# Kernel optimization log

Hardware: AMD Instinct MI355X
Metric: run time of the kernel (lower is better)

Reference implementation:

```python
import jax, jax.numpy as jnp
import numpy as np

B, T, L, H, I, W_OUT = 64, 512, 2, 512, 128, 32


def setup_inputs() -> dict:
    key = jax.random.key(0)
    ks = jax.random.split(key, 12)
    stdv = 1.0 / np.sqrt(H)
    u = lambda k, shape: jax.random.uniform(k, shape, jnp.float32, -stdv, stdv)
    return {
        "x": jax.random.normal(ks[0], (B, T, I), jnp.float32),
        "noise": jax.random.normal(ks[1], (B, T, L, H), jnp.float32) * 0.1,
        "W_ih0": u(ks[2], (H, I)),
        "W_ih1": u(ks[3], (H, H)),
        "W_hh0": u(ks[4], (H, H)),
        "W_hh1": u(ks[5], (H, H)),
        "b_ih0": u(ks[6], (H,)),
        "b_ih1": u(ks[7], (H,)),
        "b_hh0": u(ks[8], (H,)),
        "b_hh1": u(ks[9], (H,)),
        "fc_w": u(ks[10], (W_OUT, H)),
        "fc_b": u(ks[11], (W_OUT,)),
    }


def reference(x, noise, W_ih0, W_ih1, W_hh0, W_hh1, b_ih0, b_ih1, b_hh0, b_hh1, fc_w, fc_b):
    # Sequential two-layer tanh RNN; scan over time keeps hidden state resident.
    h0 = jnp.zeros((B, H), x.dtype)
    h1 = jnp.zeros((B, H), x.dtype)

    def step(carry, inp):
        h0, h1 = carry
        x_t, n_t = inp  # x_t: [B,I], n_t: [B,L,H]
        h0 = jnp.tanh(x_t @ W_ih0.T + b_ih0 + h0 @ W_hh0.T + b_hh0 + n_t[:, 0, :])
        h1 = jnp.tanh(h0 @ W_ih1.T + b_ih1 + h1 @ W_hh1.T + b_hh1 + n_t[:, 1, :])
        return (h0, h1), None

    # time-major scan inputs
    (h0, h1), _ = jax.lax.scan(step, (h0, h1), (jnp.swapaxes(x, 0, 1), jnp.swapaxes(noise, 0, 1)))
    return h1 @ fc_w.T + fc_b  # [B, wheel_len]
```

## Files before the change

kernel.cpp:

```cpp
#include <hip/hip_runtime.h>


#define T_STEPS 512
#define NBATCH  64
#define DRING   32
#define THR_LEAD 20

typedef _Float16 half2v __attribute__((ext_vector_type(2)));
typedef _Float16 f16x8  __attribute__((ext_vector_type(8)));
typedef float    f32x4  __attribute__((ext_vector_type(4)));

__device__ __forceinline__ unsigned pack2(float a, float b) {
    _Float16 fa = (_Float16)a, fb = (_Float16)b;
    unsigned short ua = __builtin_bit_cast(unsigned short, fa);
    unsigned short ub = __builtin_bit_cast(unsigned short, fb);
    return (unsigned)ua | ((unsigned)ub << 16);
}

__device__ __forceinline__ float fast_tanh(float xv) {
    float e2 = __builtin_amdgcn_exp2f(xv * 2.885390082f);
    return 1.f - 2.f * __builtin_amdgcn_rcpf(e2 + 1.f);
}

__device__ __forceinline__ f32x4 mfma16(uint4 a, uint4 b, f32x4 c) {
    return __builtin_amdgcn_mfma_f32_16x16x32_f16(
        __builtin_bit_cast(f16x8, a), __builtin_bit_cast(f16x8, b), c, 0, 0, 0);
}

__device__ __forceinline__ void bar_lgkm() {
    asm volatile("s_waitcnt lgkmcnt(0)\n\ts_barrier" ::: "memory");
}

__device__ __forceinline__ float ntload_f(const float* p) {
    return __builtin_nontemporal_load(p);
}
__device__ __forceinline__ float2 ntload_f2(const float* p) {
    float a = __builtin_nontemporal_load(p);
    float b = __builtin_nontemporal_load(p + 1);
    return make_float2(a, b);
}

__device__ __forceinline__ unsigned poll1(unsigned long long* p, unsigned tag,
                                          long& budget) {
    unsigned long long v = __hip_atomic_load(p, __ATOMIC_RELAXED, __HIP_MEMORY_SCOPE_AGENT);
    while ((unsigned)(v >> 32) != tag && budget > 0) {
        v = __hip_atomic_load(p, __ATOMIC_RELAXED, __HIP_MEMORY_SCOPE_AGENT);
        --budget;
    }
    return (unsigned)v;
}

__device__ __forceinline__ unsigned poll_spec(unsigned long long* p,
                                              unsigned long long* sent,
                                              unsigned tag, long& budget) {
    unsigned long long v  = __hip_atomic_load(p,    __ATOMIC_RELAXED, __HIP_MEMORY_SCOPE_AGENT);
    unsigned long long sv = __hip_atomic_load(sent, __ATOMIC_RELAXED, __HIP_MEMORY_SCOPE_AGENT);
    while ((unsigned)(sv >> 32) != tag && budget > 0) {
        __builtin_amdgcn_s_sleep(1);
        v  = __hip_atomic_load(p,    __ATOMIC_RELAXED, __HIP_MEMORY_SCOPE_AGENT);
        sv = __hip_atomic_load(sent, __ATOMIC_RELAXED, __HIP_MEMORY_SCOPE_AGENT);
        --budget;
    }
    if ((unsigned)(v >> 32) == tag) return (unsigned)v;
    return poll1(p, tag, budget);
}

#define NWPF (4 * 16 * 16 * 64)

__global__ void init_pack(const float* __restrict__ Wih0, const float* __restrict__ Whh0,
                          const float* __restrict__ Wih1, const float* __restrict__ Whh1,
                          uint4* __restrict__ wp0, uint4* __restrict__ wp1,
                          int* __restrict__ prog) {
    int gid = blockIdx.x * 256 + threadIdx.x;
    if (gid == 32) prog[32] = prog[32] + 1;
    if (gid < 32) prog[gid] = 0;
    if (gid < NWPF) {
        int lane = gid & 63, f = (gid >> 6) & 15, w = (gid >> 10) & 15, s = gid >> 14;
        uint4 o = make_uint4(0, 0, 0, 0);
        if (w < 10) {
            int rt = f >> 1, ktl = f & 1;
            int r = s * 128 + rt * 16 + (lane & 15);
            unsigned dv[4];
#pragma unroll
            for (int d = 0; d < 4; ++d) {
                int kp = 32 * w + ktl * 16 + ((lane >> 4) * 4) + d;
                float w0, w1;
                if (kp < 64) { w0 = Wih0[r * 128 + 2 * kp]; w1 = Wih0[r * 128 + 2 * kp + 1]; }
                else { int p0 = kp - 64;
                       w0 = Whh0[r * 512 + 2 * p0]; w1 = Whh0[r * 512 + 2 * p0 + 1]; }
                dv[d] = pack2(w0, w1);
            }
            o = make_uint4(dv[0], dv[1], dv[2], dv[3]);
        }
        wp0[gid] = o;
    } else if (gid < 2 * NWPF) {
        int idx = gid - NWPF;
        int lane = idx & 63, f = (idx >> 6) & 15, w = (idx >> 10) & 15, s = idx >> 14;
        int rt = f >> 1, ktl = f & 1;
        int r = s * 128 + rt * 16 + (lane & 15);
        unsigned dv[4];
#pragma unroll
        for (int d = 0; d < 4; ++d) {
            int kp = 32 * w + ktl * 16 + ((lane >> 4) * 4) + d;
            float w0, w1;
            if (kp < 256) { w0 = Wih1[r * 512 + 2 * kp]; w1 = Wih1[r * 512 + 2 * kp + 1]; }
            else { int p1 = kp - 256;
                   w0 = Whh1[r * 512 + 2 * p1]; w1 = Whh1[r * 512 + 2 * p1 + 1]; }
            dv[d] = pack2(w0, w1);
        }
        wp1[idx] = make_uint4(dv[0], dv[1], dv[2], dv[3]);
    }
}

template <int LAYER>
__device__ __forceinline__ void run_layer(
    int b0, int s, int L, int pair,
    const float* __restrict__ x, const float* __restrict__ noise,
    const uint4* __restrict__ wp,
    const float* __restrict__ bih, const float* __restrict__ bhh,
    unsigned long long* __restrict__ hb0, unsigned long long* __restrict__ hb1,
    int* __restrict__ prog,
    const float* __restrict__ fcw, const float* __restrict__ fcb,
    float* __restrict__ out) {
    constexpr int NP = (LAYER == 0) ? 10 : 16;

    const int w = L >> 6, lane = L & 63;
    const int j31 = lane & 31, bbl = lane >> 5;
    const unsigned tagbase = ((unsigned)prog[32]) << 10;
    long budget = 2000000000L;

    const bool active = (LAYER == 1) || (w < 10);
    const bool isX    = (LAYER == 0) && (w < 2);
    const bool isPF   = (LAYER == 1) && (w < 8);
    const bool isPoll = (LAYER == 0) ? (w >= 2 && w < 10) : (w >= 8);

    uint4 wfr[16];
#pragma unroll
    for (int f = 0; f < 16; ++f) {
        wfr[f] = wp[(size_t)(((s * 16 + w) * 16) + f) * 64 + lane];
        asm volatile("" : "+v"(wfr[f].x), "+v"(wfr[f].y), "+v"(wfr[f].z), "+v"(wfr[f].w));
    }

    __shared__ __align__(16) unsigned strip[16][64];
    __shared__ __align__(16) float psum[2][NP][2][128];
    for (int i = L; i < 16 * 64; i += 1024) ((unsigned*)strip)[i] = 0u;

    const bool isRed = (LAYER == 0) ? (L >= 640 && L < 896) : (L < 256);
    const int ur  = (LAYER == 0) ? (L - 640) : L;
    const int bbr = (ur >> 7) & 1, rw = ur & 127;
    const int rgl = s * 128 + rw;
    float cb = 0.f, nz = 0.f;
    if (isRed) {
        cb = bih[rgl] + bhh[rgl];
        nz = ntload_f(&noise[(((size_t)(b0 + bbr) * T_STEPS + 0) * 2 + LAYER) * 512 + rgl]);
    }
    __syncthreads();

    unsigned long long pf = 0;
    float2 xf = make_float2(0.f, 0.f);
    if constexpr (LAYER == 1) {
        if (isPF) {
            unsigned long long* sb = &hb0[((size_t)0 * NBATCH + (b0 + bbl)) * 256 + 32 * w];
            unsigned v = poll_spec(sb + j31, sb + 31, tagbase + 1, budget);
            pf = ((unsigned long long)(tagbase + 1) << 32) | v;
        }
    } else {
        if (isX)
            xf = ntload_f2(x + ((size_t)(b0 + bbl) * T_STEPS + 0) * 128 + 2 * (32 * w + j31));
    }

    int known = 0;
    const int colm = lane & 15, kg = lane >> 4;

    for (int t = 0; t < T_STEPS; ++t) {
        const int p = t & 1;
        const bool last = (t == T_STEPS - 1);
        __builtin_amdgcn_s_setprio(1);

        if constexpr (LAYER == 1) {
            if (isPF) {
                unsigned want = tagbase + (unsigned)t + 1;
                if ((unsigned)(pf >> 32) != want) {
                    __builtin_amdgcn_s_setprio(0);
                    unsigned long long* sb =
                        &hb0[((size_t)(t & (DRING - 1)) * NBATCH + (b0 + bbl)) * 256 + 32 * w];
                    unsigned v = poll_spec(sb + j31, sb + 31, want, budget);
                    pf = ((unsigned long long)want << 32) | v;
                    __builtin_amdgcn_s_setprio(1);
                }
                strip[w][bbl * 32 + j31] = (unsigned)pf;
                if (!last)
                    pf = __hip_atomic_load(&hb0[((size_t)((t + 1) & (DRING - 1)) * NBATCH +
                                                 (b0 + bbl)) * 256 + (32 * w + j31)],
                                           __ATOMIC_RELAXED, __HIP_MEMORY_SCOPE_AGENT);
            } else {
                if (t > 0) {
                    unsigned long long* sb =
                        &hb1[((size_t)((t - 1) & 3) * NBATCH + (b0 + bbl)) * 256 + 32 * (w - 8)];
                    __builtin_amdgcn_s_setprio(0);
                    unsigned v = poll_spec(sb + j31, sb + 31, tagbase + (unsigned)t, budget);
                    __builtin_amdgcn_s_setprio(1);
                    strip[w][bbl * 32 + j31] = v;
                }
            }
        } else {
            if (isX) {
                strip[w][bbl * 32 + j31] = pack2(xf.x, xf.y);
                if (!last)
                    xf = ntload_f2(x + ((size_t)(b0 + bbl) * T_STEPS + (t + 1)) * 128 +
                                   2 * (32 * w + j31));
            } else if (isPoll) {
                if (t > 0) {
                    unsigned long long* sb =
                        &hb0[((size_t)((t - 1) & (DRING - 1)) * NBATCH + (b0 + bbl)) * 256 +
                             (32 * w - 64)];
                    __builtin_amdgcn_s_setprio(0);
                    unsigned v = poll_spec(sb + j31, sb + 31, tagbase + (unsigned)t, budget);
                    __builtin_amdgcn_s_setprio(1);
                    strip[w][bbl * 32 + j31] = v;
                }
            }
        }

        float nznext = 0.f;
        if (!last && isRed)
            nznext = ntload_f(&noise[(((size_t)(b0 + bbr) * T_STEPS + (t + 1)) * 2 + LAYER) * 512 + rgl]);

        if (active) {
            const unsigned* sb = &strip[w][(colm & 1) * 32 + kg * 4];
            uint4 B0 = *(const uint4*)&sb[0];
            uint4 B1 = *(const uint4*)&sb[16];
#pragma unroll
            for (int rt = 0; rt < 8; ++rt) {
                f32x4 C = {0.f, 0.f, 0.f, 0.f};
                C = mfma16(wfr[2 * rt + 0], B0, C);
                C = mfma16(wfr[2 * rt + 1], B1, C);
                if (colm < 2)
                    *(f32x4*)&psum[p][w][colm][rt * 16 + 4 * kg] = C;
            }
        }

        bar_lgkm();

        if (isRed) {
            float sum = 0.f;
#pragma unroll
            for (int g = 0; g < NP; ++g) sum += psum[p][g][bbr][rw];
            float h = fast_tanh(sum + cb + nz);
            float hnb = __shfl_down(h, 1);
            if ((ur & 1) == 0) {
                unsigned pv = pack2(h, hnb);
                int pr = s * 64 + (rw >> 1);
                unsigned long long atom =
                    ((unsigned long long)(tagbase + (unsigned)t + 1) << 32) |
                    (unsigned long long)pv;
                if constexpr (LAYER == 0) {
                    if (t - known > THR_LEAD) {
                        __builtin_amdgcn_s_setprio(0);
                        while (t - known > THR_LEAD && budget > 0) {
                            __builtin_amdgcn_s_sleep(2);
                            known = __hip_atomic_load(&prog[pair], __ATOMIC_RELAXED,
                                                      __HIP_MEMORY_SCOPE_AGENT);
                            --budget;
                        }
                        __builtin_amdgcn_s_setprio(1);
                    }
                    __hip_atomic_store(&hb0[((size_t)(t & (DRING - 1)) * NBATCH + (b0 + bbr)) * 256 + pr],
                                       atom, __ATOMIC_RELAXED, __HIP_MEMORY_SCOPE_AGENT);
                } else {
                    __hip_atomic_store(&hb1[((size_t)(t & 3) * NBATCH + (b0 + bbr)) * 256 + pr],
                                       atom, __ATOMIC_RELAXED, __HIP_MEMORY_SCOPE_AGENT);
                }
            }
            nz = nznext;
        }
        if constexpr (LAYER == 1) {
            if (s == 0 && L == 960 && t > 1)
                __hip_atomic_store(&prog[pair], t - 2, __ATOMIC_RELAXED,
                                   __HIP_MEMORY_SCOPE_AGENT);
        }
        __builtin_amdgcn_s_setprio(0);
    }

    if constexpr (LAYER == 1) {
        if (s == 0) {
            __syncthreads();
            float* hsbuf = (float*)&psum[0][0][0][0];
            float* partb = hsbuf + 1024;
            if (L < 512) {
                int bl = L >> 8, pr = L & 255;
                unsigned v = poll1(&hb1[((size_t)((T_STEPS - 1) & 3) * NBATCH + (b0 + bl)) * 256 + pr],
                                   tagbase + (unsigned)T_STEPS, budget);
                half2v h2 = __builtin_bit_cast(half2v, v);
                hsbuf[bl * 512 + 2 * pr] = (float)h2.x;
                hsbuf[bl * 512 + 2 * pr + 1] = (float)h2.y;
            }
            __syncthreads();
            {
                int bl = L >> 9, rest = L & 511, o = rest & 31, seg = rest >> 5;
                const float* wr = fcw + o * 512 + seg * 32;
                const float* hr = &hsbuf[bl * 512 + seg * 32];
                float a = 0.f;
#pragma unroll
                for (int k = 0; k < 32; ++k) a = fmaf(wr[k], hr[k], a);
                partb[bl * 512 + rest] = a;
            }
            __syncthreads();
            if (L < 64) {
                int bl = L >> 5, o = L & 31;
                float ssum = fcb[o];
#pragma unroll
                for (int sgi = 0; sgi < 16; ++sgi) ssum += partb[bl * 512 + sgi * 32 + o];
                out[(b0 + bl) * 32 + o] = ssum;
            }
        }
    }
}

__global__ __launch_bounds__(1024, 4)
void rnn_dual(const float* __restrict__ x, const float* __restrict__ noise,
              const uint4* __restrict__ wp0, const uint4* __restrict__ wp1,
              const float* __restrict__ bih0, const float* __restrict__ bhh0,
              const float* __restrict__ bih1, const float* __restrict__ bhh1,
              const float* __restrict__ fcw, const float* __restrict__ fcb,
              unsigned long long* __restrict__ hb0,
              unsigned long long* __restrict__ hb1,
              int* __restrict__ prog,
              float* __restrict__ out) {
    const int L = threadIdx.x;
    const int gid = blockIdx.x;
    const int cl = gid & 63;
    const int s = gid >> 6;
    const int layer = cl >> 5;
    const int pair = cl & 31;
    const int b0 = pair * 2;
    if (layer == 0)
        run_layer<0>(b0, s, L, pair, x, noise, wp0, bih0, bhh0,
                     hb0, hb1, prog, nullptr, nullptr, nullptr);
    else
        run_layer<1>(b0, s, L, pair, x, noise, wp1, bih1, bhh1,
                     hb0, hb1, prog, fcw, fcb, out);
}

extern "C" void kernel_launch(void* const* d_in, const int* in_sizes, int n_in,
                              void* d_out, int out_size, void* d_ws, size_t ws_size,
                              hipStream_t stream) {
    const float* x     = (const float*)d_in[0];
    const float* noise = (const float*)d_in[1];
    const float* Wih0  = (const float*)d_in[2];
    const float* Wih1  = (const float*)d_in[3];
    const float* Whh0  = (const float*)d_in[4];
    const float* Whh1  = (const float*)d_in[5];
    const float* bih0  = (const float*)d_in[6];
    const float* bih1  = (const float*)d_in[7];
    const float* bhh0  = (const float*)d_in[8];
    const float* bhh1  = (const float*)d_in[9];
    const float* fcw   = (const float*)d_in[10];
    const float* fcb   = (const float*)d_in[11];
    float* out = (float*)d_out;

    char* ws = (char*)d_ws;
    size_t o = 0;
    uint4* wp0 = (uint4*)(ws + o); o += (size_t)NWPF * 16;
    uint4* wp1 = (uint4*)(ws + o); o += (size_t)NWPF * 16;
    unsigned long long* hb0 = (unsigned long long*)(ws + o);
    o += (size_t)DRING * NBATCH * 256 * 8;
    unsigned long long* hb1 = (unsigned long long*)(ws + o);
    o += (size_t)4 * NBATCH * 256 * 8;
    int* prog = (int*)(ws + o); o += 33 * sizeof(int);

    const int total = 2 * NWPF;
    init_pack<<<(total + 255) / 256, 256, 0, stream>>>(Wih0, Whh0, Wih1, Whh1,
                                                       wp0, wp1, prog);
    rnn_dual<<<256, 1024, 0, stream>>>(x, noise, wp0, wp1, bih0, bhh0, bih1, bhh1,
                                       fcw, fcb, hb0, hb1, prog, out);
}
```

Measured before the change: 1.155 ms.

## Feed locally produced hidden slice via LDS instead of polling global ring

Each block now writes its own freshly computed hidden-state slice directly into the shared-memory strip. The waves that own that slice no longer poll the global ring buffer for it; only waves covering other blocks' slices still poll. This removes a global round-trip and spin-wait from the critical path for the local slice. To stay correct it adds a second barrier per timestep and drops the double-buffered psum, which adds barrier cost in exchange.

```diff
diff --git a/kernel.cpp b/kernel.cpp
--- a/kernel.cpp
+++ b/kernel.cpp
@@ -129,10 +129,12 @@
     const unsigned tagbase = ((unsigned)prog[32]) << 10;
     long budget = 2000000000L;
 
-    const bool active = (LAYER == 1) || (w < 10);
-    const bool isX    = (LAYER == 0) && (w < 2);
-    const bool isPF   = (LAYER == 1) && (w < 8);
-    const bool isPoll = (LAYER == 0) ? (w >= 2 && w < 10) : (w >= 8);
+    const bool active   = (LAYER == 1) || (w < 10);
+    const bool isX      = (LAYER == 0) && (w < 2);
+    const bool isPF     = (LAYER == 1) && (w < 8);
+    const bool isOwn    = (LAYER == 0) ? (w == 2 + 2 * s || w == 3 + 2 * s)
+                                       : (w == 8 + 2 * s || w == 9 + 2 * s);
+    const bool isRemote = active && !isX && !isPF && !isOwn;
 
     uint4 wfr[16];
 #pragma unroll
@@ -142,7 +144,7 @@
     }
 
     __shared__ __align__(16) unsigned strip[16][64];
-    __shared__ __align__(16) float psum[2][NP][2][128];
+    __shared__ __align__(16) float psum[NP][2][128];
     for (int i = L; i < 16 * 64; i += 1024) ((unsigned*)strip)[i] = 0u;
 
     const bool isRed = (LAYER == 0) ? (L >= 640 && L < 896) : (L < 256);
@@ -173,7 +175,6 @@
     const int colm = lane & 15, kg = lane >> 4;
 
     for (int t = 0; t < T_STEPS; ++t) {
-        const int p = t & 1;
         const bool last = (t == T_STEPS - 1);
         __builtin_amdgcn_s_setprio(1);
 
@@ -193,7 +194,7 @@
                     pf = __hip_atomic_load(&hb0[((size_t)((t + 1) & (DRING - 1)) * NBATCH +
                                                  (b0 + bbl)) * 256 + (32 * w + j31)],
                                            __ATOMIC_RELAXED, __HIP_MEMORY_SCOPE_AGENT);
-            } else {
+            } else if (isRemote) {
                 if (t > 0) {
                     unsigned long long* sb =
                         &hb1[((size_t)((t - 1) & 3) * NBATCH + (b0 + bbl)) * 256 + 32 * (w - 8)];
@@ -209,7 +210,7 @@
                 if (!last)
                     xf = ntload_f2(x + ((size_t)(b0 + bbl) * T_STEPS + (t + 1)) * 128 +
                                    2 * (32 * w + j31));
-            } else if (isPoll) {
+            } else if (isRemote) {
                 if (t > 0) {
                     unsigned long long* sb =
                         &hb0[((size_t)((t - 1) & (DRING - 1)) * NBATCH + (b0 + bbl)) * 256 +
@@ -236,7 +237,7 @@
                 C = mfma16(wfr[2 * rt + 0], B0, C);
                 C = mfma16(wfr[2 * rt + 1], B1, C);
                 if (colm < 2)
-                    *(f32x4*)&psum[p][w][colm][rt * 16 + 4 * kg] = C;
+                    *(f32x4*)&psum[w][colm][rt * 16 + 4 * kg] = C;
             }
         }
 
@@ -245,7 +246,7 @@
         if (isRed) {
             float sum = 0.f;
 #pragma unroll
-            for (int g = 0; g < NP; ++g) sum += psum[p][g][bbr][rw];
+            for (int g = 0; g < NP; ++g) sum += psum[g][bbr][rw];
             float h = fast_tanh(sum + cb + nz);
             float hnb = __shfl_down(h, 1);
             if ((ur & 1) == 0) {
@@ -267,9 +268,11 @@
                     }
                     __hip_atomic_store(&hb0[((size_t)(t & (DRING - 1)) * NBATCH + (b0 + bbr)) * 256 + pr],
                                        atom, __ATOMIC_RELAXED, __HIP_MEMORY_SCOPE_AGENT);
+                    strip[2 + (pr >> 5)][bbr * 32 + (pr & 31)] = pv;
                 } else {
                     __hip_atomic_store(&hb1[((size_t)(t & 3) * NBATCH + (b0 + bbr)) * 256 + pr],
                                        atom, __ATOMIC_RELAXED, __HIP_MEMORY_SCOPE_AGENT);
+                    strip[8 + (pr >> 5)][bbr * 32 + (pr & 31)] = pv;
                 }
             }
             nz = nznext;
@@ -279,38 +282,37 @@
                 __hip_atomic_store(&prog[pair], t - 2, __ATOMIC_RELAXED,
                                    __HIP_MEMORY_SCOPE_AGENT);
         }
+        bar_lgkm();
         __builtin_amdgcn_s_setprio(0);
     }
 
     if constexpr (LAYER == 1) {
         if (s == 0) {
-            __syncthreads();
-            float* hsbuf = (float*)&psum[0][0][0][0];
-            float* partb = hsbuf + 1024;
+            __shared__ float hs[2][512];
+            __shared__ float part[2][512];
             if (L < 512) {
                 int bl = L >> 8, pr = L & 255;
                 unsigned v = poll1(&hb1[((size_t)((T_STEPS - 1) & 3) * NBATCH + (b0 + bl)) * 256 + pr],
                                    tagbase + (unsigned)T_STEPS, budget);
                 half2v h2 = __builtin_bit_cast(half2v, v);
-                hsbuf[bl * 512 + 2 * pr] = (float)h2.x;
-                hsbuf[bl * 512 + 2 * pr + 1] = (float)h2.y;
+                hs[bl][2 * pr] = (float)h2.x; hs[bl][2 * pr + 1] = (float)h2.y;
             }
             __syncthreads();
             {
                 int bl = L >> 9, rest = L & 511, o = rest & 31, seg = rest >> 5;
                 const float* wr = fcw + o * 512 + seg * 32;
-                const float* hr = &hsbuf[bl * 512 + seg * 32];
+                const float* hr = &hs[bl][seg * 32];
                 float a = 0.f;
 #pragma unroll
                 for (int k = 0; k < 32; ++k) a = fmaf(wr[k], hr[k], a);
-                partb[bl * 512 + rest] = a;
+                part[bl][rest] = a;
             }
             __syncthreads();
             if (L < 64) {
                 int bl = L >> 5, o = L & 31;
                 float ssum = fcb[o];
 #pragma unroll
-                for (int sgi = 0; sgi < 16; ++sgi) ssum += partb[bl * 512 + sgi * 32 + o];
+                for (int sgi = 0; sgi < 16; ++sgi) ssum += part[bl][sgi * 32 + o];
                 out[(b0 + bl) * 32 + o] = ssum;
             }
         }
```

Measured after the change: 1.132 ms. 1.02x faster.
